# Kernel optimization log

Measured on AMD Instinct MI355X. Metric: run time of the kernel, lower is better.

The kernel has to match this reference:

```python
import jax, jax.numpy as jnp
import numpy as np

TAU = 2.0
BN_EPS = 1e-5
HEADS = 8

# spikingjelly-style Heaviside spike with sigmoid surrogate gradient (alpha=4)
@jax.custom_vjp
def spike(x):
    return (x >= 0.0).astype(x.dtype)

def _spike_fwd(x):
    return (x >= 0.0).astype(x.dtype), x

def _spike_bwd(x, g):
    s = jax.nn.sigmoid(4.0 * x)
    return (g * 4.0 * s * (1.0 - s),)

spike.defvjp(_spike_fwd, _spike_bwd)

def lif(x, thresh):
    """Multi-step LIF (tau=2, decay_input=True, hard reset to 0, detach_reset).
    x: (T, ...) input current; returns spikes of the same shape."""
    def step(v, xt):
        v = v + (xt - v) / TAU          # charge
        s = spike(v - thresh)           # fire
        v = v * (1.0 - jax.lax.stop_gradient(s))  # hard reset, detached
        return v, s
    _, s = jax.lax.scan(step, jnp.zeros_like(x[0]), x)
    return s

def bn(x, gamma, beta, mean, var):
    # inference-mode BatchNorm2d over channel axis 2 of (T,B,C,H,W)
    sh = (1, 1, -1, 1, 1)
    scale = gamma / jnp.sqrt(var + BN_EPS)
    return (x - mean.reshape(sh)) * scale.reshape(sh) + beta.reshape(sh)

def setup_inputs() -> dict:
    key = jax.random.key(0)
    T, B, C, H, W = 4, 16, 512, 16, 16
    ks = jax.random.split(key, 24)
    def wmat(k):
        return jax.random.normal(k, (C, C), jnp.float32) * (1.0 / np.sqrt(C))
    def bnp(k):
        k1, k2, k3, k4 = jax.random.split(k, 4)
        return (jax.random.normal(k1, (C,), jnp.float32) * 0.1 + 1.0,
                jax.random.normal(k2, (C,), jnp.float32) * 0.1,
                jax.random.normal(k3, (C,), jnp.float32) * 0.1,
                jax.random.uniform(k4, (C,), jnp.float32) + 0.5)
    qg, qb, qm, qvar = bnp(ks[1]); kg, kb, km, kvar = bnp(ks[3])
    vg, vb, vm, vvar = bnp(ks[5]); pg, pb, pm, pvar = bnp(ks[8])
    return {
        'x': jax.random.normal(ks[0], (T, B, C, H, W), jnp.float32),
        'wq': wmat(ks[10]), 'qg': qg, 'qb': qb, 'qm': qm, 'qvar': qvar,
        'wk': wmat(ks[11]), 'kg': kg, 'kb': kb, 'km': km, 'kvar': kvar,
        'wv': wmat(ks[12]), 'vg': vg, 'vb': vb, 'vm': vm, 'vvar': vvar,
        'wp': wmat(ks[13]), 'bp': jax.random.normal(ks[14], (C,), jnp.float32) * 0.02,
        'pg': pg, 'pb': pb, 'pm': pm, 'pvar': pvar,
    }

def reference(x, wq, qg, qb, qm, qvar, wk, kg, kb, km, kvar,
              wv, vg, vb, vm, vvar, wp, bp, pg, pb, pm, pvar):
    T, B, C, H, W = x.shape
    dh = C // HEADS
    N = H * W
    identity = x
    xs = lif(x, 1.0)  # shortcut_lif

    def branch(w, g, b, m, v):
        y = jnp.einsum('tbchw,oc->tbohw', xs, w)  # 1x1 conv, no bias
        return lif(bn(y, g, b, m, v), 1.0)

    # (T,B,C,H,W) spikes -> (T,B,heads,N,dh)
    def to_heads(s):
        return s.reshape(T, B, HEADS, dh, N).transpose(0, 1, 2, 4, 3)

    q = to_heads(branch(wq, qg, qb, qm, qvar))
    k = to_heads(branch(wk, kg, kb, km, kvar))
    v = to_heads(branch(wv, vg, vb, vm, vvar))

    kv = (k * v).sum(axis=3, keepdims=True)   # sum over tokens N -> (T,B,h,1,dh)
    kv = lif(kv, 0.5)                          # talking_heads_lif (v_threshold=0.5)

    out = q * kv                               # (T,B,h,N,dh)
    out = out.transpose(0, 1, 2, 4, 3).reshape(T, B, C, H, W)
    out = jnp.einsum('tbchw,oc->tbohw', out, wp) + bp.reshape(1, 1, -1, 1, 1)
    out = bn(out, pg, pb, pm, pvar) + identity
    return out, v
```

## Files before the change

kernel.cpp:

```cpp
#include <hip/hip_runtime.h>
#include <hip/hip_bf16.h>

typedef unsigned short u16;
typedef unsigned int u32;
typedef __attribute__((ext_vector_type(8))) short bh8;
typedef __attribute__((ext_vector_type(4))) short sh4;
typedef __attribute__((ext_vector_type(4))) float f4;

#define T_   4
#define B_   16
#define C_   512
#define N_   256
#define M2_  4096

__device__ __forceinline__ u16 f2bf(float f) {
  u32 u = __float_as_uint(f);
  u32 r = (u + 0x7FFFu + ((u >> 16) & 1u)) >> 16;
  return (u16)r;
}
__device__ __forceinline__ void gl_lds16(const void* g, void* l) {
  __builtin_amdgcn_global_load_lds(
      (const __attribute__((address_space(1))) unsigned int*)g,
      (__attribute__((address_space(3))) unsigned int*)l, 16, 0, 0);
}

__global__ void k_prep_lif(const float* __restrict__ x, u16* __restrict__ xs,
                           const float* __restrict__ wq, const float* __restrict__ wk,
                           const float* __restrict__ wv, const float* __restrict__ wp,
                           const float* qg, const float* qb, const float* qm, const float* qv,
                           const float* kg, const float* kb, const float* km, const float* kv2,
                           const float* vg, const float* vb, const float* vm, const float* vv,
                           const float* pg, const float* pb, const float* pm, const float* pv,
                           const float* bp,
                           u16* __restrict__ wcat, u16* __restrict__ wpcat,
                           float* bns, float* pss) {
  __shared__ u16 sp[4][64][68];
  int bid = blockIdx.x;
  int tid = threadIdx.x;
  if (bid < 512) {
    int b = bid >> 5, c0 = ((bid >> 2) & 7) * 64, n0 = (bid & 3) * 64;
    int rq = tid >> 4;
    int n4 = (tid & 15) * 4;
    f4 xr[4][4];
#pragma unroll
    for (int t = 0; t < 4; t++) {
      const float* xb = x + (((size_t)t * 16 + b) * 512 + c0) * 256 + n0;
#pragma unroll
      for (int i = 0; i < 4; i++)
        xr[t][i] = *(const f4*)(xb + (size_t)(rq + i * 16) * 256 + n4);
    }
    float v[16];
#pragma unroll
    for (int i = 0; i < 16; i++) v[i] = 0.f;
#pragma unroll
    for (int t = 0; t < 4; t++) {
#pragma unroll
      for (int i = 0; i < 4; i++) {
        int row = rq + i * 16;
        sh4 sv;
#pragma unroll
        for (int j = 0; j < 4; j++) {
          float vv2 = v[i * 4 + j];
          vv2 = vv2 + (xr[t][i][j] - vv2) * 0.5f;
          u16 s = 0;
          if (vv2 >= 1.0f) { s = 0x3F80; vv2 = 0.f; }
          v[i * 4 + j] = vv2;
          sv[j] = (short)s;
        }
        *(sh4*)&sp[t][row][n4] = sv;
      }
    }
    __syncthreads();
    int cp = (tid & 31) * 2;
    int nq = tid >> 5;
    for (int t = 0; t < 4; t++) {
      u16* ob = xs + (((size_t)t * 16 + b) * 256 + n0) * 512 + c0;
#pragma unroll
      for (int i = 0; i < 8; i++) {
        int n = nq + i * 8;
        u32 w = (u32)sp[t][cp][n] | ((u32)sp[t][cp + 1][n] << 16);
        *(u32*)(ob + (size_t)n * 512 + cp) = w;
      }
    }
  } else {
    int id = (bid - 512) * 256 + tid;
    if (id < 1048576) {
      int mat = id >> 18;
      int rc  = id & 262143;
      int o = rc >> 9, c = rc & 511;
      const float* src = (mat == 0) ? wq : (mat == 1) ? wk : (mat == 2) ? wv : wp;
      float w = src[rc];
      u16 hu = f2bf(w);
      float hf = __uint_as_float(((u32)hu) << 16);
      u16 lu = f2bf(w - hf);
      if (mat < 3) {
        int rI = (o >> 5) * 96 + mat * 32 + (o & 31);
        size_t base = (size_t)rI * 1024 + c;
        wcat[base] = hu; wcat[base + 512] = lu;
      } else {
        size_t base = (size_t)o * 1024 + c;
        wpcat[base] = hu; wpcat[base + 512] = lu;
      }
    } else {
      int j = id - 1048576;
      if (j < 1536) {
        int br = j >> 9, o = j & 511;
        const float *g, *b, *m, *va;
        if (br == 0)      { g = qg; b = qb; m = qm; va = qv; }
        else if (br == 1) { g = kg; b = kb; m = km; va = kv2; }
        else              { g = vg; b = vb; m = vm; va = vv; }
        float s = g[o] / sqrtf(va[o] + 1e-5f);
        int rI = (o >> 5) * 96 + br * 32 + (o & 31);
        bns[rI * 4 + 0] = s; bns[rI * 4 + 1] = m[o]; bns[rI * 4 + 2] = b[o];
        bns[rI * 4 + 3] = 0.f;
      } else if (j < 2048) {
        int c = j - 1536;
        float s = pg[c] / sqrtf(pv[c] + 1e-5f);
        pss[c * 4 + 0] = bp[c]; pss[c * 4 + 1] = pm[c];
        pss[c * 4 + 2] = s;     pss[c * 4 + 3] = pb[c];
      }
    }
  }
}

__launch_bounds__(256, 2)
__global__ void k_qkv_gemm(const u16* __restrict__ xs, const u16* __restrict__ wcat,
                           const float* __restrict__ bns,
                           u16* __restrict__ qs, float* __restrict__ vout,
                           int* __restrict__ kvp) {
  __shared__ char lds[81920];
  int tid = threadIdx.x, lane = tid & 63;
  int wr = tid >> 6;
  int lr = lane & 15, lq = lane >> 4;
  int m0 = blockIdx.x * 128;
  int cb = blockIdx.y;
  int o0 = cb * 96;
  int b = m0 >> 8, n0 = m0 & 255, half = (m0 >> 7) & 1;

  float scl[6], mn[6], bt[6];
#pragma unroll
  for (int ni = 0; ni < 6; ni++) {
    int rI = o0 + ni * 16 + lr;
    scl[ni] = bns[rI * 4]; mn[ni] = bns[rI * 4 + 1]; bt[ni] = bns[rI * 4 + 2];
  }

  int srow = tid >> 3;
  u32 sgoff = (u32)(((tid & 7) ^ (srow & 7)) << 4);
  u32 ldst = (u32)tid * 16;

  u32 aoff[2], boff[6];
#pragma unroll
  for (int mi = 0; mi < 2; mi++) {
    int r = wr * 32 + mi * 16 + lr;
    aoff[mi] = r * 128 + ((lq ^ (r & 7)) << 4);
  }
#pragma unroll
  for (int ni = 0; ni < 6; ni++) {
    int r = ni * 16 + lr;
    boff[ni] = r * 128 + ((lq ^ (r & 7)) << 4);
  }

  const char* Bb = (const char*)wcat + (size_t)o0 * 2048;

  auto STAGE = [&](int buf, int step) {
    int t = step >> 3;
    u32 kb = (u32)(step & 7) * 128;
    const char* Ab = (const char*)xs + ((size_t)t * M2_ + m0) * 1024;
    char* L = lds + buf * 40960;
#pragma unroll
    for (int r2 = 0; r2 < 4; r2++)
      gl_lds16(Ab + (size_t)(r2 * 32 + srow) * 1024 + kb + sgoff, L + r2 * 4096 + ldst);
#pragma unroll
    for (int r2 = 0; r2 < 3; r2++) {
      gl_lds16(Bb + (size_t)(r2 * 32 + srow) * 2048 + kb + sgoff, L + 16384 + r2 * 4096 + ldst);
      gl_lds16(Bb + (size_t)(r2 * 32 + srow) * 2048 + 1024 + kb + sgoff, L + 28672 + r2 * 4096 + ldst);
    }
  };

  float vst[2][6][4];
#pragma unroll
  for (int a = 0; a < 2; a++)
#pragma unroll
    for (int bq = 0; bq < 6; bq++)
#pragma unroll
      for (int c = 0; c < 4; c++) vst[a][bq][c] = 0.f;

  f4 acc[2][6];
  STAGE(0, 0);
  __syncthreads();
  int cur = 0;
  for (int step = 0; step < 32; ++step) {
    int ks = step & 7;
    if (ks == 0) {
#pragma unroll
      for (int a = 0; a < 2; a++)
#pragma unroll
        for (int bq = 0; bq < 6; bq++) { acc[a][bq][0] = 0.f; acc[a][bq][1] = 0.f; acc[a][bq][2] = 0.f; acc[a][bq][3] = 0.f; }
    }
    if (step < 31) STAGE(cur ^ 1, step + 1);
    const char* L = lds + cur * 40960;
#pragma unroll
    for (int h = 0; h < 2; h++) {
      u32 hx = (u32)h << 6;
      bh8 af[2], bf[6], lf[6];
#pragma unroll
      for (int mi = 0; mi < 2; mi++)
        af[mi] = *(const bh8*)(L + (aoff[mi] ^ hx));
#pragma unroll
      for (int ni = 0; ni < 6; ni++) {
        bf[ni] = *(const bh8*)(L + 16384 + (boff[ni] ^ hx));
        lf[ni] = *(const bh8*)(L + 28672 + (boff[ni] ^ hx));
      }
#pragma unroll
      for (int mi = 0; mi < 2; mi++)
#pragma unroll
        for (int ni = 0; ni < 6; ni++)
          acc[mi][ni] = __builtin_amdgcn_mfma_f32_16x16x32_bf16(af[mi], bf[ni], acc[mi][ni], 0, 0, 0);
#pragma unroll
      for (int mi = 0; mi < 2; mi++)
#pragma unroll
        for (int ni = 0; ni < 6; ni++)
          acc[mi][ni] = __builtin_amdgcn_mfma_f32_16x16x32_bf16(af[mi], lf[ni], acc[mi][ni], 0, 0, 0);
    }
    asm volatile("s_waitcnt vmcnt(0)" ::: "memory");
    __builtin_amdgcn_s_barrier();
    cur ^= 1;
    if (ks == 7) {
      int t = step >> 3;
      unsigned char* vbuf = (unsigned char*)(lds + (cur ^ 1) * 40960);
      short* cbuf = (short*)(lds + (cur ^ 1) * 40960 + 4096);
      int cnt0 = 0, cnt1 = 0;
      u16 kbits[2]; kbits[0] = 0; kbits[1] = 0;
#pragma unroll
      for (int ni = 0; ni < 6; ni++) {
#pragma unroll
        for (int mi = 0; mi < 2; mi++) {
#pragma unroll
          for (int j = 0; j < 4; j++) {
            float y = (acc[mi][ni][j] - mn[ni]) * scl[ni] + bt[ni];
            float vv = vst[mi][ni][j];
            vv = vv + (y - vv) * 0.5f;
            int s = (vv >= 1.0f) ? 1 : 0;
            if (s) vv = 0.f;
            vst[mi][ni][j] = vv;
            int jj = ni & 1;
            if (ni < 2) {
              int rg = m0 + wr * 32 + mi * 16 + lq * 4 + j;
              int cc = cb * 32 + jj * 16 + lr;
              qs[((size_t)t * M2_ + rg) * 512 + cc] = s ? (u16)0x3F80 : (u16)0;
            } else if (ni < 4) {
              kbits[mi] |= (u16)(s << (jj * 4 + j));
            } else {
              int row = wr * 32 + mi * 16 + lq * 4 + j;
              vbuf[row * 32 + jj * 16 + lr] = (unsigned char)s;
              int kbit = (kbits[mi] >> (jj * 4 + j)) & 1;
              if (jj == 0) cnt0 += (s & kbit); else cnt1 += (s & kbit);
            }
          }
        }
      }
      cbuf[tid * 2] = (short)cnt0; cbuf[tid * 2 + 1] = (short)cnt1;
      asm volatile("s_waitcnt lgkmcnt(0)" ::: "memory");
      __builtin_amdgcn_s_barrier();
      __builtin_amdgcn_sched_barrier(0);
      {
        int d0 = (cb & 1) * 32;
        int hh = cb >> 1;
        float* vo = vout + (((size_t)(t * 16 + b) * 8 + hh) * 256 + n0) * 64 + d0;
#pragma unroll
        for (int p = 0; p < 4; p++) {
          int row = (tid >> 3) + p * 32;
          const unsigned char* src = vbuf + row * 32 + (tid & 7) * 4;
          f4 w2; w2[0] = src[0]; w2[1] = src[1]; w2[2] = src[2]; w2[3] = src[3];
          *(f4*)(vo + (size_t)row * 64 + (tid & 7) * 4) = w2;
        }
        if (tid < 32) {
          int lr2 = tid & 15, jj = tid >> 4;
          int ssum = 0;
#pragma unroll
          for (int w3 = 0; w3 < 4; w3++)
#pragma unroll
            for (int q3 = 0; q3 < 4; q3++)
              ssum += cbuf[(w3 * 64 + q3 * 16 + lr2) * 2 + jj];
          kvp[(((t * 16 + b) * 2 + half) << 9) + cb * 32 + jj * 16 + lr2] = ssum;
        }
      }
      asm volatile("s_waitcnt lgkmcnt(0)" ::: "memory");
      __builtin_amdgcn_s_barrier();
      __builtin_amdgcn_sched_barrier(0);
    }
  }
}

__global__ void k_tlif(const int* __restrict__ kvp, unsigned char* __restrict__ mask) {
  int id = blockIdx.x * 256 + threadIdx.x;
  int b = id >> 9, c = id & 511;
  float v = 0.f;
  for (int t = 0; t < 4; t++) {
    int tb = t * 16 + b;
    int s = kvp[((tb * 2) << 9) + c] + kvp[((tb * 2 + 1) << 9) + c];
    float xx = (float)s;
    v = v + (xx - v) * 0.5f;
    unsigned char sp = 0;
    if (v >= 0.5f) { sp = 1; v = 0.f; }
    mask[tb * 512 + c] = sp;
  }
}

__launch_bounds__(256, 2)
__global__ void k_proj_gemm(const u16* __restrict__ qs, const unsigned char* __restrict__ mask,
                            const u16* __restrict__ wpc, const float* __restrict__ pss,
                            const float* __restrict__ x, float* __restrict__ out) {
  __shared__ char lds[66560];
  u16* lm = (u16*)(lds + 65536);
  int tid = threadIdx.x, lane = tid & 63, wid = tid >> 6;
  int wr = wid >> 1, wc = wid & 1, lr = lane & 15, lq = lane >> 4;
  int m0 = blockIdx.x * 128, o0 = blockIdx.y * 64;
  int tb = m0 >> 8;

  lm[tid]       = mask[tb * 512 + tid]       ? (u16)0xFFFF : (u16)0;
  lm[tid + 256] = mask[tb * 512 + tid + 256] ? (u16)0xFFFF : (u16)0;

  int srow = tid >> 3;
  u32 sgoff = (u32)(((tid & 7) ^ (srow & 7)) << 4);
  u32 ldst = (u32)tid * 16;

  u32 aoff[4], boff[2];
#pragma unroll
  for (int mi = 0; mi < 4; mi++) {
    int r = wr * 64 + mi * 16 + lr;
    aoff[mi] = r * 128 + ((lq ^ (r & 7)) << 4);
  }
#pragma unroll
  for (int ni = 0; ni < 2; ni++) {
    int r = wc * 32 + ni * 16 + lr;
    boff[ni] = r * 128 + ((lq ^ (r & 7)) << 4);
  }

  const char* Ab = (const char*)qs + (size_t)m0 * 1024;
  const char* Bb = (const char*)wpc + (size_t)o0 * 2048;

  auto STAGE = [&](int buf, int step) {
    u32 kb = (u32)step * 128;
    char* L = lds + buf * 32768;
#pragma unroll
    for (int r2 = 0; r2 < 4; r2++)
      gl_lds16(Ab + (size_t)(r2 * 32 + srow) * 1024 + kb + sgoff, L + r2 * 4096 + ldst);
#pragma unroll
    for (int r2 = 0; r2 < 2; r2++) {
      gl_lds16(Bb + (size_t)(r2 * 32 + srow) * 2048 + kb + sgoff, L + 16384 + r2 * 4096 + ldst);
      gl_lds16(Bb + (size_t)(r2 * 32 + srow) * 2048 + 1024 + kb + sgoff, L + 24576 + r2 * 4096 + ldst);
    }
  };

  f4 acc[4][2];
#pragma unroll
  for (int a = 0; a < 4; a++)
#pragma unroll
    for (int b2 = 0; b2 < 2; b2++) { acc[a][b2][0] = 0.f; acc[a][b2][1] = 0.f; acc[a][b2][2] = 0.f; acc[a][b2][3] = 0.f; }

  STAGE(0, 0);
  __syncthreads();
  int cur = 0;
  for (int step = 0; step < 8; ++step) {
    u32 kb = (u32)step * 128;
    if (step < 7) STAGE(cur ^ 1, step + 1);
    const char* L = lds + cur * 32768;
#pragma unroll
    for (int h = 0; h < 2; h++) {
      u32 hx = (u32)h << 6;
      bh8 mq = *(const bh8*)((const char*)lm + kb + (h << 6) + lq * 16);
      bh8 af[4], bf[2], lf[2];
#pragma unroll
      for (int mi = 0; mi < 4; mi++) {
        af[mi] = *(const bh8*)(L + (aoff[mi] ^ hx));
        af[mi] = af[mi] & mq;
      }
#pragma unroll
      for (int ni = 0; ni < 2; ni++) {
        bf[ni] = *(const bh8*)(L + 16384 + (boff[ni] ^ hx));
        lf[ni] = *(const bh8*)(L + 24576 + (boff[ni] ^ hx));
      }
#pragma unroll
      for (int mi = 0; mi < 4; mi++)
#pragma unroll
        for (int ni = 0; ni < 2; ni++)
          acc[mi][ni] = __builtin_amdgcn_mfma_f32_16x16x32_bf16(af[mi], bf[ni], acc[mi][ni], 0, 0, 0);
#pragma unroll
      for (int mi = 0; mi < 4; mi++)
#pragma unroll
        for (int ni = 0; ni < 2; ni++)
          acc[mi][ni] = __builtin_amdgcn_mfma_f32_16x16x32_bf16(af[mi], lf[ni], acc[mi][ni], 0, 0, 0);
    }
    asm volatile("s_waitcnt vmcnt(0)" ::: "memory");
    __builtin_amdgcn_s_barrier();
    cur ^= 1;
  }
#pragma unroll
  for (int mi = 0; mi < 4; mi++)
#pragma unroll
    for (int ni = 0; ni < 2; ni++) {
      int o = o0 + wc * 32 + ni * 16 + lr;
      f4 ps = *(const f4*)&pss[o * 4];
      int n = (m0 & 255) + wr * 64 + mi * 16 + lq * 4;
      size_t idx = (size_t)tb * 131072 + (size_t)o * 256 + n;
      f4 xv = *(const f4*)&x[idx];
      f4 res;
#pragma unroll
      for (int j = 0; j < 4; j++) {
        float u = acc[mi][ni][j] + ps[0];
        u = (u - ps[1]) * ps[2] + ps[3];
        res[j] = u + xv[j];
      }
      *(f4*)&out[idx] = res;
    }
}

extern "C" void kernel_launch(void* const* d_in, const int* in_sizes, int n_in,
                              void* d_out, int out_size, void* d_ws, size_t ws_size,
                              hipStream_t stream) {
  const float* x  = (const float*)d_in[0];
  const float* wq = (const float*)d_in[1];
  const float* qg = (const float*)d_in[2];
  const float* qb = (const float*)d_in[3];
  const float* qm = (const float*)d_in[4];
  const float* qv = (const float*)d_in[5];
  const float* wk = (const float*)d_in[6];
  const float* kg = (const float*)d_in[7];
  const float* kb = (const float*)d_in[8];
  const float* km = (const float*)d_in[9];
  const float* kv = (const float*)d_in[10];
  const float* wv = (const float*)d_in[11];
  const float* vg = (const float*)d_in[12];
  const float* vb = (const float*)d_in[13];
  const float* vm = (const float*)d_in[14];
  const float* vv = (const float*)d_in[15];
  const float* wp = (const float*)d_in[16];
  const float* bp = (const float*)d_in[17];
  const float* pg = (const float*)d_in[18];
  const float* pb = (const float*)d_in[19];
  const float* pm = (const float*)d_in[20];
  const float* pv = (const float*)d_in[21];

  char* w = (char*)d_ws;
  u16*  XS    = (u16*)(w + 0);
  u16*  QS    = (u16*)(w + 16777216);
  u16*  WCAT  = (u16*)(w + 33554432);
  u16*  WPCAT = (u16*)(w + 36700160);
  float* BNS  = (float*)(w + 37748736);
  float* PSS  = (float*)(w + 37773312);
  int*   KVP  = (int*)(w + 37781504);
  unsigned char* MASK = (unsigned char*)(w + 38043648);

  float* out  = (float*)d_out;
  float* vout = out + 8388608;

  k_prep_lif<<<4616, 256, 0, stream>>>(x, XS, wq, wk, wv, wp,
                                       qg, qb, qm, qv, kg, kb, km, kv,
                                       vg, vb, vm, vv, pg, pb, pm, pv, bp,
                                       WCAT, WPCAT, BNS, PSS);
  k_qkv_gemm<<<dim3(32, 16), 256, 0, stream>>>(XS, WCAT, BNS, QS, vout, KVP);
  k_tlif<<<32, 256, 0, stream>>>(KVP, MASK);
  k_proj_gemm<<<dim3(128, 8), 256, 0, stream>>>(QS, MASK, WPCAT, PSS, x, out);
}
```

Baseline: 203.2 us.

## Split K across waves in QKV GEMM and fold talking-heads LIF into projection

The QKV GEMM now gives each wave a 64-row M tile and one half of each 128-wide K slice (split-K across wave pairs), so A and B fragments are reused over more MFMAs per LDS read. Partial sums are reduced through LDS at the end of each timestep, and only half the waves then run the BN/LIF epilogue. The separate talking-heads LIF kernel is removed: every projection block recomputes the 4-step LIF mask from the kv partial counts, which saves a launch but repeats that small recurrence in each block. The trade-offs are more accumulator registers (96 floats) and extra barriers during the epilogue reduction.

```diff
diff --git a/kernel.cpp b/kernel.cpp
--- a/kernel.cpp
+++ b/kernel.cpp
@@ -130,34 +130,28 @@
                            int* __restrict__ kvp) {
   __shared__ char lds[81920];
   int tid = threadIdx.x, lane = tid & 63;
-  int wr = tid >> 6;
+  int wid = tid >> 6;
+  int mw = wid & 1, kw = wid >> 1;
   int lr = lane & 15, lq = lane >> 4;
   int m0 = blockIdx.x * 128;
   int cb = blockIdx.y;
   int o0 = cb * 96;
   int b = m0 >> 8, n0 = m0 & 255, half = (m0 >> 7) & 1;
 
-  float scl[6], mn[6], bt[6];
-#pragma unroll
-  for (int ni = 0; ni < 6; ni++) {
-    int rI = o0 + ni * 16 + lr;
-    scl[ni] = bns[rI * 4]; mn[ni] = bns[rI * 4 + 1]; bt[ni] = bns[rI * 4 + 2];
-  }
-
   int srow = tid >> 3;
   u32 sgoff = (u32)(((tid & 7) ^ (srow & 7)) << 4);
   u32 ldst = (u32)tid * 16;
 
-  u32 aoff[2], boff[6];
-#pragma unroll
-  for (int mi = 0; mi < 2; mi++) {
-    int r = wr * 32 + mi * 16 + lr;
-    aoff[mi] = r * 128 + ((lq ^ (r & 7)) << 4);
+  u32 aoff[4], boff[6];
+#pragma unroll
+  for (int mi = 0; mi < 4; mi++) {
+    int r = mw * 64 + mi * 16 + lr;
+    aoff[mi] = r * 128 + (((lq ^ (r & 7)) ^ (kw << 2)) << 4);
   }
 #pragma unroll
   for (int ni = 0; ni < 6; ni++) {
     int r = ni * 16 + lr;
-    boff[ni] = r * 128 + ((lq ^ (r & 7)) << 4);
+    boff[ni] = r * 128 + (((lq ^ (r & 7)) ^ (kw << 2)) << 4);
   }
 
   const char* Bb = (const char*)wcat + (size_t)o0 * 2048;
@@ -177,15 +171,15 @@
     }
   };
 
-  float vst[2][6][4];
-#pragma unroll
-  for (int a = 0; a < 2; a++)
+  float vst[4][6][4];
+#pragma unroll
+  for (int a = 0; a < 4; a++)
 #pragma unroll
     for (int bq = 0; bq < 6; bq++)
 #pragma unroll
       for (int c = 0; c < 4; c++) vst[a][bq][c] = 0.f;
 
-  f4 acc[2][6];
+  f4 acc[4][6];
   STAGE(0, 0);
   __syncthreads();
   int cur = 0;
@@ -193,76 +187,98 @@
     int ks = step & 7;
     if (ks == 0) {
 #pragma unroll
-      for (int a = 0; a < 2; a++)
+      for (int a = 0; a < 4; a++)
 #pragma unroll
         for (int bq = 0; bq < 6; bq++) { acc[a][bq][0] = 0.f; acc[a][bq][1] = 0.f; acc[a][bq][2] = 0.f; acc[a][bq][3] = 0.f; }
     }
     if (step < 31) STAGE(cur ^ 1, step + 1);
     const char* L = lds + cur * 40960;
-#pragma unroll
-    for (int h = 0; h < 2; h++) {
-      u32 hx = (u32)h << 6;
-      bh8 af[2], bf[6], lf[6];
-#pragma unroll
-      for (int mi = 0; mi < 2; mi++)
-        af[mi] = *(const bh8*)(L + (aoff[mi] ^ hx));
-#pragma unroll
-      for (int ni = 0; ni < 6; ni++) {
-        bf[ni] = *(const bh8*)(L + 16384 + (boff[ni] ^ hx));
-        lf[ni] = *(const bh8*)(L + 28672 + (boff[ni] ^ hx));
-      }
-#pragma unroll
-      for (int mi = 0; mi < 2; mi++)
-#pragma unroll
-        for (int ni = 0; ni < 6; ni++)
-          acc[mi][ni] = __builtin_amdgcn_mfma_f32_16x16x32_bf16(af[mi], bf[ni], acc[mi][ni], 0, 0, 0);
-#pragma unroll
-      for (int mi = 0; mi < 2; mi++)
-#pragma unroll
-        for (int ni = 0; ni < 6; ni++)
-          acc[mi][ni] = __builtin_amdgcn_mfma_f32_16x16x32_bf16(af[mi], lf[ni], acc[mi][ni], 0, 0, 0);
+    bh8 af[4];
+#pragma unroll
+    for (int mi = 0; mi < 4; mi++)
+      af[mi] = *(const bh8*)(L + aoff[mi]);
+#pragma unroll
+    for (int ni = 0; ni < 6; ni++) {
+      bh8 bf = *(const bh8*)(L + 16384 + boff[ni]);
+      bh8 lf = *(const bh8*)(L + 28672 + boff[ni]);
+#pragma unroll
+      for (int mi = 0; mi < 4; mi++)
+        acc[mi][ni] = __builtin_amdgcn_mfma_f32_16x16x32_bf16(af[mi], bf, acc[mi][ni], 0, 0, 0);
+#pragma unroll
+      for (int mi = 0; mi < 4; mi++)
+        acc[mi][ni] = __builtin_amdgcn_mfma_f32_16x16x32_bf16(af[mi], lf, acc[mi][ni], 0, 0, 0);
     }
     asm volatile("s_waitcnt vmcnt(0)" ::: "memory");
     __builtin_amdgcn_s_barrier();
     cur ^= 1;
     if (ks == 7) {
       int t = step >> 3;
-      unsigned char* vbuf = (unsigned char*)(lds + (cur ^ 1) * 40960);
-      short* cbuf = (short*)(lds + (cur ^ 1) * 40960 + 4096);
-      int cnt0 = 0, cnt1 = 0;
-      u16 kbits[2]; kbits[0] = 0; kbits[1] = 0;
-#pragma unroll
-      for (int ni = 0; ni < 6; ni++) {
-#pragma unroll
-        for (int mi = 0; mi < 2; mi++) {
-#pragma unroll
-          for (int j = 0; j < 4; j++) {
-            float y = (acc[mi][ni][j] - mn[ni]) * scl[ni] + bt[ni];
-            float vv = vst[mi][ni][j];
-            vv = vv + (y - vv) * 0.5f;
-            int s = (vv >= 1.0f) ? 1 : 0;
-            if (s) vv = 0.f;
-            vst[mi][ni][j] = vv;
-            int jj = ni & 1;
-            if (ni < 2) {
-              int rg = m0 + wr * 32 + mi * 16 + lq * 4 + j;
-              int cc = cb * 32 + jj * 16 + lr;
-              qs[((size_t)t * M2_ + rg) * 512 + cc] = s ? (u16)0x3F80 : (u16)0;
-            } else if (ni < 4) {
-              kbits[mi] |= (u16)(s << (jj * 4 + j));
-            } else {
-              int row = wr * 32 + mi * 16 + lq * 4 + j;
-              vbuf[row * 32 + jj * 16 + lr] = (unsigned char)s;
-              int kbit = (kbits[mi] >> (jj * 4 + j)) & 1;
-              if (jj == 0) cnt0 += (s & kbit); else cnt1 += (s & kbit);
+      char* dead = lds + (cur ^ 1) * 40960;
+#pragma unroll
+      for (int p = 0; p < 2; p++) {
+        if (kw == 1) {
+#pragma unroll
+          for (int m2 = 0; m2 < 2; m2++)
+#pragma unroll
+            for (int ni = 0; ni < 6; ni++)
+              *(f4*)(dead + (((mw * 12 + m2 * 6 + ni) * 64 + lane) << 4)) = acc[p * 2 + m2][ni];
+        }
+        asm volatile("s_waitcnt lgkmcnt(0)" ::: "memory");
+        __builtin_amdgcn_s_barrier();
+        if (kw == 0) {
+#pragma unroll
+          for (int m2 = 0; m2 < 2; m2++)
+#pragma unroll
+            for (int ni = 0; ni < 6; ni++) {
+              f4 o = *(const f4*)(dead + (((mw * 12 + m2 * 6 + ni) * 64 + lane) << 4));
+              acc[p * 2 + m2][ni][0] += o[0];
+              acc[p * 2 + m2][ni][1] += o[1];
+              acc[p * 2 + m2][ni][2] += o[2];
+              acc[p * 2 + m2][ni][3] += o[3];
+            }
+        }
+        asm volatile("s_waitcnt lgkmcnt(0)" ::: "memory");
+        __builtin_amdgcn_s_barrier();
+      }
+      unsigned char* vbuf = (unsigned char*)dead;
+      short* cbuf = (short*)(dead + 4096);
+      if (kw == 0) {
+        int cnt0 = 0, cnt1 = 0;
+        u16 kbits[4]; kbits[0] = 0; kbits[1] = 0; kbits[2] = 0; kbits[3] = 0;
+#pragma unroll
+        for (int ni = 0; ni < 6; ni++) {
+          int rI = o0 + ni * 16 + lr;
+          f4 bn4 = *(const f4*)&bns[rI * 4];
+          int jj = ni & 1;
+#pragma unroll
+          for (int mi = 0; mi < 4; mi++) {
+#pragma unroll
+            for (int j = 0; j < 4; j++) {
+              float y = (acc[mi][ni][j] - bn4[1]) * bn4[0] + bn4[2];
+              float vv = vst[mi][ni][j];
+              vv = vv + (y - vv) * 0.5f;
+              int s = (vv >= 1.0f) ? 1 : 0;
+              if (s) vv = 0.f;
+              vst[mi][ni][j] = vv;
+              if (ni < 2) {
+                int rg = m0 + mw * 64 + mi * 16 + lq * 4 + j;
+                int cc = cb * 32 + jj * 16 + lr;
+                qs[((size_t)t * M2_ + rg) * 512 + cc] = s ? (u16)0x3F80 : (u16)0;
+              } else if (ni < 4) {
+                kbits[mi] |= (u16)(s << (jj * 4 + j));
+              } else {
+                int row = mw * 64 + mi * 16 + lq * 4 + j;
+                vbuf[row * 32 + jj * 16 + lr] = (unsigned char)s;
+                int kbit = (kbits[mi] >> (jj * 4 + j)) & 1;
+                if (jj == 0) cnt0 += (s & kbit); else cnt1 += (s & kbit);
+              }
             }
           }
         }
-      }
-      cbuf[tid * 2] = (short)cnt0; cbuf[tid * 2 + 1] = (short)cnt1;
+        cbuf[tid * 2] = (short)cnt0; cbuf[tid * 2 + 1] = (short)cnt1;
+      }
       asm volatile("s_waitcnt lgkmcnt(0)" ::: "memory");
       __builtin_amdgcn_s_barrier();
-      __builtin_amdgcn_sched_barrier(0);
       {
         int d0 = (cb & 1) * 32;
         int hh = cb >> 1;
@@ -278,7 +294,7 @@
           int lr2 = tid & 15, jj = tid >> 4;
           int ssum = 0;
 #pragma unroll
-          for (int w3 = 0; w3 < 4; w3++)
+          for (int w3 = 0; w3 < 2; w3++)
 #pragma unroll
             for (int q3 = 0; q3 < 4; q3++)
               ssum += cbuf[(w3 * 64 + q3 * 16 + lr2) * 2 + jj];
@@ -287,28 +303,12 @@
       }
       asm volatile("s_waitcnt lgkmcnt(0)" ::: "memory");
       __builtin_amdgcn_s_barrier();
-      __builtin_amdgcn_sched_barrier(0);
-    }
-  }
-}
-
-__global__ void k_tlif(const int* __restrict__ kvp, unsigned char* __restrict__ mask) {
-  int id = blockIdx.x * 256 + threadIdx.x;
-  int b = id >> 9, c = id & 511;
-  float v = 0.f;
-  for (int t = 0; t < 4; t++) {
-    int tb = t * 16 + b;
-    int s = kvp[((tb * 2) << 9) + c] + kvp[((tb * 2 + 1) << 9) + c];
-    float xx = (float)s;
-    v = v + (xx - v) * 0.5f;
-    unsigned char sp = 0;
-    if (v >= 0.5f) { sp = 1; v = 0.f; }
-    mask[tb * 512 + c] = sp;
+    }
   }
 }
 
 __launch_bounds__(256, 2)
-__global__ void k_proj_gemm(const u16* __restrict__ qs, const unsigned char* __restrict__ mask,
+__global__ void k_proj_gemm(const u16* __restrict__ qs, const int* __restrict__ kvp,
                             const u16* __restrict__ wpc, const float* __restrict__ pss,
                             const float* __restrict__ x, float* __restrict__ out) {
   __shared__ char lds[66560];
@@ -318,8 +318,24 @@
   int m0 = blockIdx.x * 128, o0 = blockIdx.y * 64;
   int tb = m0 >> 8;
 
-  lm[tid]       = mask[tb * 512 + tid]       ? (u16)0xFFFF : (u16)0;
-  lm[tid + 256] = mask[tb * 512 + tid + 256] ? (u16)0xFFFF : (u16)0;
+  {
+    int b_ = tb & 15, tt = tb >> 4;
+#pragma unroll
+    for (int ci = 0; ci < 2; ci++) {
+      int cc = tid + ci * 256;
+      float v = 0.f; u16 mk = 0;
+#pragma unroll
+      for (int t2 = 0; t2 < 4; t2++) {
+        int tb2 = t2 * 16 + b_;
+        int s = kvp[((tb2 * 2) << 9) + cc] + kvp[((tb2 * 2 + 1) << 9) + cc];
+        v = v + ((float)s - v) * 0.5f;
+        int sp = (v >= 0.5f) ? 1 : 0;
+        if (sp) v = 0.f;
+        if (t2 == tt) mk = sp ? (u16)0xFFFF : (u16)0;
+      }
+      lm[cc] = mk;
+    }
+  }
 
   int srow = tid >> 3;
   u32 sgoff = (u32)(((tid & 7) ^ (srow & 7)) << 4);
@@ -450,7 +466,6 @@
   float* BNS  = (float*)(w + 37748736);
   float* PSS  = (float*)(w + 37773312);
   int*   KVP  = (int*)(w + 37781504);
-  unsigned char* MASK = (unsigned char*)(w + 38043648);
 
   float* out  = (float*)d_out;
   float* vout = out + 8388608;
@@ -460,6 +475,5 @@
                                        vg, vb, vm, vv, pg, pb, pm, pv, bp,
                                        WCAT, WPCAT, BNS, PSS);
   k_qkv_gemm<<<dim3(32, 16), 256, 0, stream>>>(XS, WCAT, BNS, QS, vout, KVP);
-  k_tlif<<<32, 256, 0, stream>>>(KVP, MASK);
-  k_proj_gemm<<<dim3(128, 8), 256, 0, stream>>>(QS, MASK, WPCAT, PSS, x, out);
-}
+  k_proj_gemm<<<dim3(128, 8), 256, 0, stream>>>(QS, KVP, WPCAT, PSS, x, out);
+}
```

Result: slower. 239.1 us (+17.6%).
